# Performance work log

Hardware: AMD Instinct MI355X
Metric: run time of the kernel (lower is better)

Reference implementation:

```python
import jax, jax.numpy as jnp
import numpy as np

D = 128          # embed_d
T = 10           # MAX_NEIGHBORS
L = 2            # n_layers
B = 4096
ND, FD = 20000, 2048
NG, FG = 20000, 1024
NC, FC = 10000, 512


def setup_inputs() -> dict:
    key = jax.random.key(0)
    ks = jax.random.split(key, 18)
    inp = {
        'drug_feats': jax.random.normal(ks[0], (ND, FD), jnp.float32),
        'gene_feats': jax.random.normal(ks[1], (NG, FG), jnp.float32),
        'cell_feats': jax.random.normal(ks[2], (NC, FC), jnp.float32),
        'Wd': jax.random.normal(ks[3], (FD, D), jnp.float32) / np.sqrt(FD),
        'bd': jnp.zeros((D,), jnp.float32),
        'Wg': jax.random.normal(ks[4], (FG, D), jnp.float32) / np.sqrt(FG),
        'bg': jnp.zeros((D,), jnp.float32),
        'Wc': jax.random.normal(ks[5], (FC, D), jnp.float32) / np.sqrt(FC),
        'bc': jnp.zeros((D,), jnp.float32),
        'gru_W': jax.random.normal(ks[6], (L, 3, D, 3 * D), jnp.float32) / np.sqrt(D),
        'gru_U': jax.random.normal(ks[7], (L, 3, D, 3 * D), jnp.float32) / np.sqrt(D),
        'gru_b': jnp.zeros((L, 3, 3 * D), jnp.float32),
        'att': jax.random.normal(ks[8], (L, 2 * D), jnp.float32) / np.sqrt(2 * D),
        'ids': jax.random.randint(ks[9], (B,), 0, ND, jnp.int32),
        # neighbor ids in [-1, N-1]; -1 == PAD_VALUE
        'neigh_drug': jax.random.randint(ks[10], (B, T), 0, ND + 1, jnp.int32) - 1,
        'neigh_gene': jax.random.randint(ks[11], (B, T), 0, NG + 1, jnp.int32) - 1,
        'neigh_cell': jax.random.randint(ks[12], (B, T), 0, NC + 1, jnp.int32) - 1,
    }
    return inp


def _proj_gather(table, W, b, idx):
    # gather raw features by id (PAD -> zeros) then project, matching
    # conteng_agg + masked scatter in node_het_agg.
    mask = (idx >= 0)                              # [B, T]
    safe = jnp.clip(idx, 0, None)
    f = table[safe] @ W + b                        # [B, T, D]
    return f * mask[..., None].astype(f.dtype), mask


def _gru_seq(x, W, U, b):
    # x: [B, T, D]; torch-style GRU, returns all hidden states [B, T, D]
    xw = jnp.einsum('btd,de->bte', x, W) + b       # [B, T, 3D]
    h0 = jnp.zeros((x.shape[0], U.shape[0]), x.dtype)

    def step(h, xt):
        hu = h @ U
        xz, xr, xn = jnp.split(xt, 3, axis=-1)
        hz, hr, hn = jnp.split(hu, 3, axis=-1)
        z = jax.nn.sigmoid(xz + hz)
        r = jax.nn.sigmoid(xr + hr)
        n = jnp.tanh(xn + r * hn)
        h = (1.0 - z) * n + z * h
        return h, h

    _, hs = jax.lax.scan(step, h0, jnp.swapaxes(xw, 0, 1))
    return jnp.swapaxes(hs, 0, 1)


def reference(drug_feats, gene_feats, cell_feats, Wd, bd, Wg, bg, Wc, bc,
              gru_W, gru_U, gru_b, att, ids, neigh_drug, neigh_gene, neigh_cell):
    # self embeddings: conteng_agg(batch_ids, drug_type)
    h = drug_feats[ids] @ Wd + bd                  # [B, D]

    # neighbor content features are the layer-0 projections every layer
    # (the torch code recomputes conteng_agg per layer; result is identical)
    neigh = [
        _proj_gather(drug_feats, Wd, bd, neigh_drug),
        _proj_gather(gene_feats, Wg, bg, neigh_gene),
        _proj_gather(cell_feats, Wc, bc, neigh_cell),
    ]

    for l in range(L):
        cands = [h]
        for t, (nf, mask) in enumerate(neigh):
            out = _gru_seq(nf, gru_W[l, t], gru_U[l, t], gru_b[l, t])  # [B,T,D]
            m = mask.astype(out.dtype)
            cnt = jnp.maximum(m.sum(-1, keepdims=True), 1.0)
            cands.append((out * m[..., None]).sum(1) / cnt)            # [B,D]
        C = jnp.stack(cands, axis=1)                                   # [B,4,D]
        cat = jnp.concatenate(
            [jnp.broadcast_to(h[:, None, :], C.shape), C], axis=-1)    # [B,4,2D]
        w = jax.nn.softmax(jax.nn.leaky_relu(cat @ att[l]), axis=-1)   # [B,4]
        h = jnp.einsum('bk,bkd->bd', w, C)
    return h
```

## Files before the change

kernel.cpp:

```cpp
#include <hip/hip_runtime.h>
#include <stdint.h>


typedef short bf16x8 __attribute__((ext_vector_type(8)));
typedef float f32x4  __attribute__((ext_vector_type(4)));

__device__ __forceinline__ short f2bf(float f) {
  union { float f; unsigned u; } v; v.f = f;
  unsigned r = (v.u + 0x7fffu + ((v.u >> 16) & 1u)) >> 16;
  return (short)r;
}
__device__ __forceinline__ float b2f(short s) {
  union { float f; unsigned u; } v; v.u = ((unsigned)(unsigned short)s) << 16;
  return v.f;
}
__device__ __forceinline__ unsigned cvt_pk_bf16(float lo, float hi) {
  unsigned r;
  asm("v_cvt_pk_bf16_f32 %0, %1, %2" : "=v"(r) : "v"(lo), "v"(hi));
  return r;
}
__device__ __forceinline__ f32x4 mfma_bf16(bf16x8 a, bf16x8 b, f32x4 c) {
  return __builtin_amdgcn_mfma_f32_16x16x32_bf16(a, b, c, 0, 0, 0);
}

struct PrepW { const float* src[3]; short* dst[3]; int K[3]; };

__global__ __launch_bounds__(256) void prep_w(PrepW a) {
  const int y = blockIdx.y;
  const int K = a.K[y];
  int i = blockIdx.x * 256 + threadIdx.x;
  if (i < K * 128) {
    int k = i >> 7, n = i & 127;
    a.dst[y][(size_t)n * K + k] = f2bf(a.src[y][i]);
  }
}

__global__ __launch_bounds__(256) void prep_gru(const float* __restrict__ W,
                                                const float* __restrict__ U,
                                                short* __restrict__ dW,
                                                short* __restrict__ dU) {
  const int y = blockIdx.y;
  const float* s = (y < 6) ? W + (size_t)y * 49152 : U + (size_t)(y - 6) * 49152;
  short* d       = (y < 6) ? dW + (size_t)y * 49152 : dU + (size_t)(y - 6) * 49152;
  int i = blockIdx.x * 256 + threadIdx.x;
  if (i < 49152) {
    int k = i / 384, n = i - k * 384;
    d[(size_t)n * 128 + k] = f2bf(s[i]);
  }
}

struct ProjA {
  const float* A[3]; const short* Wt[3]; const float* bias[3];
  short* Pb[3]; float* Pf[3]; int M[3];
};

template<int KI>
__device__ __forceinline__ void proj_body(
    const float* __restrict__ A, const short* __restrict__ Wt,
    const float* __restrict__ bias, short* __restrict__ Pb,
    float* __restrict__ Pf, int M, short (*As)[16][136]) {
  const int K  = KI << 7;
  const int m0 = blockIdx.x * 16;
  if (m0 >= M) return;
  const int tid  = threadIdx.x;
  const int lane = tid & 63;
  const int w    = tid >> 6;
  const int wc   = w * 32;
  const int quad = lane >> 4;
  const int ln   = lane & 15;
  const int kq   = quad * 8;

  const int arow = tid >> 4;
  const int akc  = (tid & 15) * 8;
  const int krot = blockIdx.x % KI;

  const float* arp  = A + (size_t)(m0 + arow) * K + akc;
  const short* brp0 = Wt + (size_t)(wc + ln) * K + kq;
  const short* brp1 = Wt + (size_t)(wc + 16 + ln) * K + kq;

  float4 ar[2][2];
  bf16x8 b0[2][4], b1[2][4];
  f32x4 acc0 = (f32x4){0.f, 0.f, 0.f, 0.f};
  f32x4 acc1 = (f32x4){0.f, 0.f, 0.f, 0.f};

  auto kof = [&](int i) {
    int ks = krot + i; if (ks >= KI) ks -= KI; return ks << 7;
  };
  auto loadA = [&](int bank, int k0) {
    const float4* p = (const float4*)(arp + k0);
    ar[bank][0] = p[0]; ar[bank][1] = p[1];
  };
  auto loadB = [&](int bank, int k0) {
#pragma unroll
    for (int kt = 0; kt < 4; kt++) {
      b0[bank][kt] = *(const bf16x8*)(brp0 + k0 + kt * 32);
      b1[bank][kt] = *(const bf16x8*)(brp1 + k0 + kt * 32);
    }
  };
  auto cvtStore = [&](int buf, int bank) {
    union { unsigned u[4]; bf16x8 v; } pk;
    pk.u[0] = cvt_pk_bf16(ar[bank][0].x, ar[bank][0].y);
    pk.u[1] = cvt_pk_bf16(ar[bank][0].z, ar[bank][0].w);
    pk.u[2] = cvt_pk_bf16(ar[bank][1].x, ar[bank][1].y);
    pk.u[3] = cvt_pk_bf16(ar[bank][1].z, ar[bank][1].w);
    *(bf16x8*)&As[buf][arow][akc] = pk.v;
  };

  loadA(0, kof(0));
  loadA(1, kof(1));
  loadB(0, kof(0));
  cvtStore(0, 0);
  __syncthreads();

#pragma unroll
  for (int i = 0; i < KI; i++) {
    if (i + 1 < KI) loadB((i + 1) & 1, kof(i + 1));
    if (i + 2 < KI) loadA(i & 1, kof(i + 2));
#pragma unroll
    for (int kt = 0; kt < 4; kt++) {
      bf16x8 af = *(const bf16x8*)&As[i & 1][ln][kt * 32 + kq];
      acc0 = mfma_bf16(af, b0[i & 1][kt], acc0);
      acc1 = mfma_bf16(af, b1[i & 1][kt], acc1);
    }
    if (i + 1 < KI) cvtStore((i + 1) & 1, (i + 1) & 1);
    __syncthreads();
  }

#pragma unroll
  for (int nj = 0; nj < 2; nj++) {
    const int col = wc + nj * 16 + ln;
    const float bv = bias[col];
#pragma unroll
    for (int r = 0; r < 4; r++) {
      const int row = m0 + quad * 4 + r;
      const float v = (nj ? acc1[r] : acc0[r]) + bv;
      if (Pb) Pb[(size_t)row * 128 + col] = f2bf(v);
      if (Pf) Pf[(size_t)row * 128 + col] = v;
    }
  }
}

__global__ __launch_bounds__(256, 4) void proj_all(ProjA p) {
  __shared__ alignas(16) short As[2][16][136];
  const int y = blockIdx.y;
  if (y == 0)
    proj_body<16>(p.A[0], p.Wt[0], p.bias[0], p.Pb[0], p.Pf[0], p.M[0], As);
  else if (y == 1)
    proj_body<8>(p.A[1], p.Wt[1], p.bias[1], p.Pb[1], p.Pf[1], p.M[1], As);
  else
    proj_body<4>(p.A[2], p.Wt[2], p.bias[2], p.Pb[2], p.Pf[2], p.M[2], As);
}

__global__ __launch_bounds__(256) void gather_h0(const float* __restrict__ Pd,
                                                 const int* __restrict__ ids,
                                                 float* __restrict__ h) {
  int i = blockIdx.x * 256 + threadIdx.x;
  int b = i >> 7, d = i & 127;
  h[i] = Pd[(size_t)ids[b] * 128 + d];
}

__global__ __launch_bounds__(256) void xw_all(
    const short* __restrict__ P0, const short* __restrict__ P1,
    const short* __restrict__ P2, const int* __restrict__ n0,
    const int* __restrict__ n1, const int* __restrict__ n2,
    const short* __restrict__ gWt_all, const float* __restrict__ grub_all,
    short* __restrict__ xwT_base, int s_base) {
  const int s  = s_base + blockIdx.z;
  const int ty = s - (s / 3) * 3;
  const short* Pb  = (ty == 0) ? P0 : (ty == 1) ? P1 : P2;
  const int*   nbr = (ty == 0) ? n0 : (ty == 1) ? n1 : n2;
  const short* Wts = gWt_all + (size_t)s * 49152;
  const float* gbs = grub_all + (size_t)s * 384;
  short* xwT = xwT_base + (size_t)blockIdx.z * 40960 * 384;

  __shared__ alignas(16) short As[64][136];
  __shared__ alignas(16) short Bs[128][136];
  const int tid  = threadIdx.x;
  const int lane = tid & 63;
  const int w    = tid >> 6;
  const int wr   = (w >> 1) * 32;
  const int wc   = (w & 1) * 64;
  const int quad = lane >> 4;
  const int ln   = lane & 15;
  const int m0    = blockIdx.x * 64;
  const int nbase = blockIdx.y * 128;

  {
    const int row = tid >> 2;
    const int kc  = (tid & 3) * 32;
    const int idx = nbr[m0 + row];
    if (idx >= 0) {
      const short* p = Pb + (size_t)idx * 128 + kc;
#pragma unroll
      for (int i = 0; i < 4; i++)
        *(bf16x8*)&As[row][kc + i * 8] = *(const bf16x8*)(p + i * 8);
    } else {
      bf16x8 zv;
#pragma unroll
      for (int i = 0; i < 8; i++) zv[i] = 0;
#pragma unroll
      for (int i = 0; i < 4; i++) *(bf16x8*)&As[row][kc + i * 8] = zv;
    }
  }
  {
    const int n  = tid >> 1;
    const int kc = (tid & 1) * 64;
    const short* p = Wts + (size_t)(nbase + n) * 128 + kc;
#pragma unroll
    for (int i = 0; i < 8; i++)
      *(bf16x8*)&Bs[n][kc + i * 8] = *(const bf16x8*)(p + i * 8);
  }
  __syncthreads();

  f32x4 acc[2][4];
#pragma unroll
  for (int i = 0; i < 2; i++)
#pragma unroll
    for (int j = 0; j < 4; j++) acc[i][j] = (f32x4){0.f, 0.f, 0.f, 0.f};

#pragma unroll
  for (int kt = 0; kt < 4; kt++) {
    bf16x8 af[2], bfr[4];
#pragma unroll
    for (int mi = 0; mi < 2; mi++)
      af[mi] = *(const bf16x8*)&As[wr + mi * 16 + ln][kt * 32 + quad * 8];
#pragma unroll
    for (int nj = 0; nj < 4; nj++)
      bfr[nj] = *(const bf16x8*)&Bs[wc + nj * 16 + ln][kt * 32 + quad * 8];
#pragma unroll
    for (int mi = 0; mi < 2; mi++)
#pragma unroll
      for (int nj = 0; nj < 4; nj++)
        acc[mi][nj] = mfma_bf16(af[mi], bfr[nj], acc[mi][nj]);
  }

#pragma unroll
  for (int mi = 0; mi < 2; mi++)
#pragma unroll
    for (int nj = 0; nj < 4; nj++) {
      const int col = wc + nj * 16 + ln;
      const float bv = gbs[nbase + col];
#pragma unroll
      for (int r = 0; r < 4; r++) {
        const int rt   = m0 + wr + mi * 16 + quad * 4 + r;
        const int grow = rt / 10;
        const int st   = rt - grow * 10;
        xwT[((size_t)st * 4096 + grow) * 384 + nbase + col] =
            f2bf(acc[mi][nj][r] + bv);
      }
    }
}

__global__ __launch_bounds__(256) void scan_all(
    const short* __restrict__ xwT_base, const short* __restrict__ Ut_base,
    const int* __restrict__ n0, const int* __restrict__ n1,
    const int* __restrict__ n2, float* __restrict__ out_base, int s_base) {
  const int sz = blockIdx.y;
  const int s  = s_base + sz;
  const int ty = s - (s / 3) * 3;
  const short* xwT = xwT_base + (size_t)sz * 40960 * 384;
  const short* Utz = Ut_base + (size_t)s * 49152;
  const int*   nbr = (ty == 0) ? n0 : (ty == 1) ? n1 : n2;
  float* outp = out_base + (size_t)sz * 4096 * 128;

  __shared__ alignas(16) short hs[16][128];
  __shared__ alignas(16) short xls[16][392];
  __shared__ float mask_s[16][10];
  __shared__ float cinv[16];

  const int tid  = threadIdx.x;
  const int lane = tid & 63;
  const int w    = tid >> 6;
  const int nb   = w * 32;
  const int quad = lane >> 4;
  const int ln   = lane & 15;
  const int r0   = blockIdx.x * 16;

  if (tid < 160) {
    int i = tid / 10, tt = tid % 10;
    mask_s[i][tt] = (nbr[(r0 + i) * 10 + tt] >= 0) ? 1.f : 0.f;
  }
  {
    short* hf = &hs[0][0];
    for (int i = tid; i < 16 * 128; i += 256) hf[i] = 0;
  }
  __syncthreads();
  if (tid < 16) {
    float sm = 0.f;
    for (int tt = 0; tt < 10; tt++) sm += mask_s[tid][tt];
    cinv[tid] = 1.f / fmaxf(sm, 1.f);
  }

  bf16x8 u[3][2][4];
#pragma unroll
  for (int g = 0; g < 3; g++)
#pragma unroll
    for (int jj = 0; jj < 2; jj++)
#pragma unroll
      for (int kt = 0; kt < 4; kt++)
        u[g][jj][kt] = *(const bf16x8*)(Utz +
            (size_t)(g * 128 + nb + jj * 16 + ln) * 128 + kt * 32 + quad * 8);

  int srow[3], scol[3];
#pragma unroll
  for (int j = 0; j < 3; j++) {
    const int o = tid * 24 + j * 8;
    srow[j] = o / 384;
    scol[j] = o - srow[j] * 384;
  }

  float hreg[2][4], oacc[2][4];
#pragma unroll
  for (int jj = 0; jj < 2; jj++)
#pragma unroll
    for (int r = 0; r < 4; r++) { hreg[jj][r] = 0.f; oacc[jj][r] = 0.f; }

  __syncthreads();

  for (int st = 0; st < 10; st++) {
    bf16x8 a[4];
#pragma unroll
    for (int kt = 0; kt < 4; kt++)
      a[kt] = *(const bf16x8*)&hs[ln][kt * 32 + quad * 8];

    const short* src = xwT + ((size_t)st * 4096 + r0) * 384;
    bf16x8 xrg[3];
#pragma unroll
    for (int j = 0; j < 3; j++)
      xrg[j] = *(const bf16x8*)(src + tid * 24 + j * 8);

    f32x4 hu[3][2];
#pragma unroll
    for (int g = 0; g < 3; g++)
#pragma unroll
      for (int jj = 0; jj < 2; jj++) hu[g][jj] = (f32x4){0.f, 0.f, 0.f, 0.f};
#pragma unroll
    for (int kt = 0; kt < 4; kt++)
#pragma unroll
      for (int g = 0; g < 3; g++)
#pragma unroll
        for (int jj = 0; jj < 2; jj++)
          hu[g][jj] = mfma_bf16(a[kt], u[g][jj][kt], hu[g][jj]);

#pragma unroll
    for (int j = 0; j < 3; j++)
      *(bf16x8*)&xls[srow[j]][scol[j]] = xrg[j];
    __syncthreads();

#pragma unroll
    for (int jj = 0; jj < 2; jj++) {
      const int col = nb + jj * 16 + ln;
#pragma unroll
      for (int r = 0; r < 4; r++) {
        const int row = quad * 4 + r;
        const float xz = b2f(xls[row][col]);
        const float xr = b2f(xls[row][col + 128]);
        const float xn = b2f(xls[row][col + 256]);
        const float zg = 1.f / (1.f + __expf(-(xz + hu[0][jj][r])));
        const float rg = 1.f / (1.f + __expf(-(xr + hu[1][jj][r])));
        const float pn = xn + rg * hu[2][jj][r];
        const float e2 = __expf(2.f * pn);
        const float n  = (e2 - 1.f) / (e2 + 1.f);
        const float hn = (1.f - zg) * n + zg * hreg[jj][r];
        hreg[jj][r] = hn;
        oacc[jj][r] += hn * mask_s[row][st];
        hs[row][col] = f2bf(hn);
      }
    }
    __syncthreads();
  }

#pragma unroll
  for (int jj = 0; jj < 2; jj++)
#pragma unroll
    for (int r = 0; r < 4; r++) {
      const int row = quad * 4 + r;
      outp[(size_t)(r0 + row) * 128 + nb + jj * 16 + ln] =
          oacc[jj][r] * cinv[row];
    }
}

__global__ __launch_bounds__(256) void attn_kernel(
    const float* __restrict__ hin, const float* __restrict__ cand,
    const float* __restrict__ att, float* __restrict__ hout) {
  const int tid  = threadIdx.x;
  const int lane = tid & 63;
  const int w    = tid >> 6;
  const int gb   = blockIdx.x * 4 + w;

  const float ah0 = att[lane],       ah1 = att[lane + 64];
  const float ac0 = att[128 + lane], ac1 = att[192 + lane];

  float c0[4], c1[4];
  c0[0] = hin[(size_t)gb * 128 + lane];
  c1[0] = hin[(size_t)gb * 128 + 64 + lane];
#pragma unroll
  for (int k = 1; k < 4; k++) {
    const float* p = cand + (size_t)(k - 1) * 4096 * 128 + (size_t)gb * 128;
    c0[k] = p[lane]; c1[k] = p[64 + lane];
  }

  float sh = ah0 * c0[0] + ah1 * c1[0];
#pragma unroll
  for (int m = 1; m < 64; m <<= 1) sh += __shfl_xor(sh, m);

  float e[4];
#pragma unroll
  for (int k = 0; k < 4; k++) {
    float sv = ac0 * c0[k] + ac1 * c1[k];
#pragma unroll
    for (int m = 1; m < 64; m <<= 1) sv += __shfl_xor(sv, m);
    sv += sh;
    e[k] = (sv > 0.f) ? sv : 0.01f * sv;
  }
  const float mx = fmaxf(fmaxf(e[0], e[1]), fmaxf(e[2], e[3]));
  float wk[4], wsum = 0.f;
#pragma unroll
  for (int k = 0; k < 4; k++) { wk[k] = __expf(e[k] - mx); wsum += wk[k]; }
  const float inv = 1.f / wsum;
  float o0 = 0.f, o1 = 0.f;
#pragma unroll
  for (int k = 0; k < 4; k++) { o0 += wk[k] * c0[k]; o1 += wk[k] * c1[k]; }
  hout[(size_t)gb * 128 + lane]      = o0 * inv;
  hout[(size_t)gb * 128 + 64 + lane] = o1 * inv;
}

extern "C" void kernel_launch(void* const* d_in, const int* in_sizes, int n_in,
                              void* d_out, int out_size, void* d_ws, size_t ws_size,
                              hipStream_t stream) {
  const float* drug = (const float*)d_in[0];
  const float* gene = (const float*)d_in[1];
  const float* cell = (const float*)d_in[2];
  const float* Wd   = (const float*)d_in[3];
  const float* bd   = (const float*)d_in[4];
  const float* Wg   = (const float*)d_in[5];
  const float* bg   = (const float*)d_in[6];
  const float* Wc   = (const float*)d_in[7];
  const float* bc   = (const float*)d_in[8];
  const float* gruW = (const float*)d_in[9];
  const float* gruU = (const float*)d_in[10];
  const float* grub = (const float*)d_in[11];
  const float* att  = (const float*)d_in[12];
  const int* ids    = (const int*)d_in[13];
  const int* nbr[3] = {(const int*)d_in[14], (const int*)d_in[15],
                       (const int*)d_in[16]};

  const size_t XW_SLOT   = (size_t)40960 * 384;
  const size_t CAND_SLOT = (size_t)4096 * 128;

  const size_t need_big =
      (size_t)20000 * 128 * 4 + (size_t)20000 * 128 * 2 +
      (size_t)20000 * 128 * 2 + (size_t)10000 * 128 * 2 +
      (size_t)4096 * 128 * 4 + 6 * CAND_SLOT * 4 + 6 * XW_SLOT * 2 +
      (size_t)2048 * 128 * 2 + (size_t)1024 * 128 * 2 + (size_t)512 * 128 * 2 +
      2 * (size_t)6 * 384 * 128 * 2 + 16384 ;
  const bool big = ws_size >= need_big;

  char* ws = (char*)d_ws;
  auto alloc = [&](size_t bytes) {
    void* p = ws; ws += (bytes + 255) & ~(size_t)255; return p;
  };
  float* Pdf  = (float*)alloc((size_t)20000 * 128 * 4);
  short* Pdb  = (short*)alloc((size_t)20000 * 128 * 2);
  short* Pgb  = (short*)alloc((size_t)20000 * 128 * 2);
  short* Pcb  = (short*)alloc((size_t)10000 * 128 * 2);
  float* h    = (float*)alloc((size_t)4096 * 128 * 4);
  float* cand = (float*)alloc((big ? 6 : 3) * CAND_SLOT * 4);
  short* xwb  = (short*)alloc((big ? 6 : 1) * XW_SLOT * 2);
  short* Wdt  = (short*)alloc((size_t)2048 * 128 * 2);
  short* Wgt  = (short*)alloc((size_t)1024 * 128 * 2);
  short* Wct  = (short*)alloc((size_t)512 * 128 * 2);
  short* gWt  = (short*)alloc((size_t)6 * 384 * 128 * 2);
  short* Ut   = (short*)alloc((size_t)6 * 384 * 128 * 2);

  {
    PrepW pw;
    pw.src[0] = Wd;  pw.dst[0] = Wdt; pw.K[0] = 2048;
    pw.src[1] = Wg;  pw.dst[1] = Wgt; pw.K[1] = 1024;
    pw.src[2] = Wc;  pw.dst[2] = Wct; pw.K[2] = 512;
    prep_w<<<dim3(1024, 3), 256, 0, stream>>>(pw);
  }
  prep_gru<<<dim3(192, 12), 256, 0, stream>>>(gruW, gruU, gWt, Ut);

  {
    ProjA pa;
    pa.A[0] = drug; pa.Wt[0] = Wdt; pa.bias[0] = bd;
    pa.Pb[0] = Pdb; pa.Pf[0] = Pdf; pa.M[0] = 20000;
    pa.A[1] = gene; pa.Wt[1] = Wgt; pa.bias[1] = bg;
    pa.Pb[1] = Pgb; pa.Pf[1] = nullptr; pa.M[1] = 20000;
    pa.A[2] = cell; pa.Wt[2] = Wct; pa.bias[2] = bc;
    pa.Pb[2] = Pcb; pa.Pf[2] = nullptr; pa.M[2] = 10000;
    proj_all<<<dim3(1250, 3), 256, 0, stream>>>(pa);
  }
  gather_h0<<<2048, 256, 0, stream>>>(Pdf, ids, h);

  if (big) {
    xw_all<<<dim3(640, 3, 6), 256, 0, stream>>>(
        Pdb, Pgb, Pcb, nbr[0], nbr[1], nbr[2], gWt, grub, xwb, 0);
    scan_all<<<dim3(256, 6), 256, 0, stream>>>(
        xwb, Ut, nbr[0], nbr[1], nbr[2], cand, 0);
    attn_kernel<<<1024, 256, 0, stream>>>(h, cand, att, h);
    attn_kernel<<<1024, 256, 0, stream>>>(
        h, cand + 3 * CAND_SLOT, att + 256, (float*)d_out);
  } else {
    for (int l = 0; l < 2; l++) {
      for (int t = 0; t < 3; t++) {
        const int s = l * 3 + t;
        xw_all<<<dim3(640, 3, 1), 256, 0, stream>>>(
            Pdb, Pgb, Pcb, nbr[0], nbr[1], nbr[2], gWt, grub, xwb, s);
        scan_all<<<dim3(256, 1), 256, 0, stream>>>(
            xwb, Ut, nbr[0], nbr[1], nbr[2], cand + (size_t)t * CAND_SLOT, s);
      }
      attn_kernel<<<1024, 256, 0, stream>>>(
          h, cand, att + l * 256, (l == 1) ? (float*)d_out : h);
    }
  }
}
```

Before: 602.5 us.

## Restructure projection GEMM to per-wave register tiles without shared memory staging

```diff
diff --git a/kernel.cpp b/kernel.cpp
--- a/kernel.cpp
+++ b/kernel.cpp
@@ -54,86 +54,61 @@
   short* Pb[3]; float* Pf[3]; int M[3];
 };
 
-template<int KI>
+template<int NC>
 __device__ __forceinline__ void proj_body(
     const float* __restrict__ A, const short* __restrict__ Wt,
     const float* __restrict__ bias, short* __restrict__ Pb,
-    float* __restrict__ Pf, int M, short (*As)[16][136]) {
-  const int K  = KI << 7;
-  const int m0 = blockIdx.x * 16;
-  if (m0 >= M) return;
+    float* __restrict__ Pf, int M) {
+  const int K    = NC * 32;
   const int tid  = threadIdx.x;
   const int lane = tid & 63;
   const int w    = tid >> 6;
-  const int wc   = w * 32;
+  const int wrow = w >> 1;
+  const int wcol = (w & 1) * 64;
   const int quad = lane >> 4;
   const int ln   = lane & 15;
   const int kq   = quad * 8;
-
-  const int arow = tid >> 4;
-  const int akc  = (tid & 15) * 8;
-  const int krot = blockIdx.x % KI;
-
-  const float* arp  = A + (size_t)(m0 + arow) * K + akc;
-  const short* brp0 = Wt + (size_t)(wc + ln) * K + kq;
-  const short* brp1 = Wt + (size_t)(wc + 16 + ln) * K + kq;
-
-  float4 ar[2][2];
-  bf16x8 b0[2][4], b1[2][4];
-  f32x4 acc0 = (f32x4){0.f, 0.f, 0.f, 0.f};
-  f32x4 acc1 = (f32x4){0.f, 0.f, 0.f, 0.f};
-
-  auto kof = [&](int i) {
-    int ks = krot + i; if (ks >= KI) ks -= KI; return ks << 7;
-  };
-  auto loadA = [&](int bank, int k0) {
-    const float4* p = (const float4*)(arp + k0);
-    ar[bank][0] = p[0]; ar[bank][1] = p[1];
-  };
-  auto loadB = [&](int bank, int k0) {
-#pragma unroll
-    for (int kt = 0; kt < 4; kt++) {
-      b0[bank][kt] = *(const bf16x8*)(brp0 + k0 + kt * 32);
-      b1[bank][kt] = *(const bf16x8*)(brp1 + k0 + kt * 32);
-    }
-  };
-  auto cvtStore = [&](int buf, int bank) {
+  const int m0   = blockIdx.x * 32 + wrow * 16;
+  if (m0 >= M) return;
+
+  const float* ap = A + (size_t)(m0 + ln) * K + kq;
+  const short* bp0 = Wt + (size_t)(wcol + ln) * K + kq;
+  const short* bp1 = bp0 + (size_t)16 * K;
+  const short* bp2 = bp0 + (size_t)32 * K;
+  const short* bp3 = bp0 + (size_t)48 * K;
+
+  f32x4 acc[4];
+#pragma unroll
+  for (int nj = 0; nj < 4; nj++) acc[nj] = (f32x4){0.f, 0.f, 0.f, 0.f};
+
+#pragma unroll 8
+  for (int c = 0; c < NC; c++) {
+    const int k0 = c * 32;
+    float4 a0 = *(const float4*)(ap + k0);
+    float4 a1 = *(const float4*)(ap + k0 + 4);
+    bf16x8 bfr0 = *(const bf16x8*)(bp0 + k0);
+    bf16x8 bfr1 = *(const bf16x8*)(bp1 + k0);
+    bf16x8 bfr2 = *(const bf16x8*)(bp2 + k0);
+    bf16x8 bfr3 = *(const bf16x8*)(bp3 + k0);
     union { unsigned u[4]; bf16x8 v; } pk;
-    pk.u[0] = cvt_pk_bf16(ar[bank][0].x, ar[bank][0].y);
-    pk.u[1] = cvt_pk_bf16(ar[bank][0].z, ar[bank][0].w);
-    pk.u[2] = cvt_pk_bf16(ar[bank][1].x, ar[bank][1].y);
-    pk.u[3] = cvt_pk_bf16(ar[bank][1].z, ar[bank][1].w);
-    *(bf16x8*)&As[buf][arow][akc] = pk.v;
-  };
-
-  loadA(0, kof(0));
-  loadA(1, kof(1));
-  loadB(0, kof(0));
-  cvtStore(0, 0);
-  __syncthreads();
-
-#pragma unroll
-  for (int i = 0; i < KI; i++) {
-    if (i + 1 < KI) loadB((i + 1) & 1, kof(i + 1));
-    if (i + 2 < KI) loadA(i & 1, kof(i + 2));
-#pragma unroll
-    for (int kt = 0; kt < 4; kt++) {
-      bf16x8 af = *(const bf16x8*)&As[i & 1][ln][kt * 32 + kq];
-      acc0 = mfma_bf16(af, b0[i & 1][kt], acc0);
-      acc1 = mfma_bf16(af, b1[i & 1][kt], acc1);
-    }
-    if (i + 1 < KI) cvtStore((i + 1) & 1, (i + 1) & 1);
-    __syncthreads();
-  }
-
-#pragma unroll
-  for (int nj = 0; nj < 2; nj++) {
-    const int col = wc + nj * 16 + ln;
+    pk.u[0] = cvt_pk_bf16(a0.x, a0.y);
+    pk.u[1] = cvt_pk_bf16(a0.z, a0.w);
+    pk.u[2] = cvt_pk_bf16(a1.x, a1.y);
+    pk.u[3] = cvt_pk_bf16(a1.z, a1.w);
+    acc[0] = mfma_bf16(pk.v, bfr0, acc[0]);
+    acc[1] = mfma_bf16(pk.v, bfr1, acc[1]);
+    acc[2] = mfma_bf16(pk.v, bfr2, acc[2]);
+    acc[3] = mfma_bf16(pk.v, bfr3, acc[3]);
+  }
+
+#pragma unroll
+  for (int nj = 0; nj < 4; nj++) {
+    const int col = wcol + nj * 16 + ln;
     const float bv = bias[col];
 #pragma unroll
     for (int r = 0; r < 4; r++) {
       const int row = m0 + quad * 4 + r;
-      const float v = (nj ? acc1[r] : acc0[r]) + bv;
+      const float v = acc[nj][r] + bv;
       if (Pb) Pb[(size_t)row * 128 + col] = f2bf(v);
       if (Pf) Pf[(size_t)row * 128 + col] = v;
     }
@@ -141,14 +116,13 @@
 }
 
 __global__ __launch_bounds__(256, 4) void proj_all(ProjA p) {
-  __shared__ alignas(16) short As[2][16][136];
   const int y = blockIdx.y;
   if (y == 0)
-    proj_body<16>(p.A[0], p.Wt[0], p.bias[0], p.Pb[0], p.Pf[0], p.M[0], As);
+    proj_body<64>(p.A[0], p.Wt[0], p.bias[0], p.Pb[0], p.Pf[0], p.M[0]);
   else if (y == 1)
-    proj_body<8>(p.A[1], p.Wt[1], p.bias[1], p.Pb[1], p.Pf[1], p.M[1], As);
+    proj_body<32>(p.A[1], p.Wt[1], p.bias[1], p.Pb[1], p.Pf[1], p.M[1]);
   else
-    proj_body<4>(p.A[2], p.Wt[2], p.bias[2], p.Pb[2], p.Pf[2], p.M[2], As);
+    proj_body<16>(p.A[2], p.Wt[2], p.bias[2], p.Pb[2], p.Pf[2], p.M[2]);
 }
 
 __global__ __launch_bounds__(256) void gather_h0(const float* __restrict__ Pd,
@@ -490,7 +464,7 @@
     pa.Pb[1] = Pgb; pa.Pf[1] = nullptr; pa.M[1] = 20000;
     pa.A[2] = cell; pa.Wt[2] = Wct; pa.bias[2] = bc;
     pa.Pb[2] = Pcb; pa.Pf[2] = nullptr; pa.M[2] = 10000;
-    proj_all<<<dim3(1250, 3), 256, 0, stream>>>(pa);
+    proj_all<<<dim3(625, 3), 256, 0, stream>>>(pa);
   }
   gather_h0<<<2048, 256, 0, stream>>>(Pdf, ids, h);
 
```

Result: slower. 653.9 us (+8.5%).
